# Kernel optimization log

Hardware: AMD Instinct MI355X
Metric: run time of the kernel (lower is better)

## Reference

```python
import jax, jax.numpy as jnp
import numpy as np

EC = 32        # pos-embed channels per coordinate (gno_embed_channels)
MAXP = 10000.0 # gno_embed_max_positions


def sin_embed(c):
    # c: [N, D] coords in [0,1] -> [N, D*EC] transformer-style sinusoidal embedding
    half = EC // 2
    freqs = MAXP ** (jnp.arange(half, dtype=jnp.float32) / half)
    ang = c[..., None] * freqs                       # [N, D, half]
    emb = jnp.concatenate([jnp.sin(ang), jnp.cos(ang)], axis=-1)  # [N, D, EC]
    return emb.reshape(c.shape[0], -1)


def mlp(h, layers):
    n = len(layers)
    for i, (W, b) in enumerate(layers):
        h = h @ W + b
        if i < n - 1:
            h = jax.nn.gelu(h)
    return h


def gno(y, xq, f_y, idx, layers, lift, reduction):
    # y: [n_y,3] source coords, xq: [n_x,3] query coords, f_y: [n_y,C_f], idx: [n_x,K]
    ye, xe = sin_embed(y), sin_embed(xq)
    K = idx.shape[1]
    ef = jnp.concatenate(
        [ye[idx], jnp.broadcast_to(xe[:, None, :], (xq.shape[0], K, xe.shape[-1]))], axis=-1)
    k = mlp(ef, layers)                              # [n_x, K, C] kernel values
    f = f_y if lift is None else f_y @ lift[0] + lift[1]
    msg = k * f[idx]                                 # gathered features modulated by kernel
    return msg.mean(axis=1) if reduction == 'mean' else msg.sum(axis=1)


def spectral_conv(v, w):
    # v: [1,X,Y,Z,C]; w: [4,m,m,m,C,C,2] (4 corner blocks, real/imag stacked)
    m = w.shape[2]
    wc = w[..., 0] + 1j * w[..., 1]
    vf = jnp.fft.rfftn(v, axes=(1, 2, 3))
    out = jnp.zeros_like(vf)
    corners = [(slice(0, m), slice(0, m)), (slice(0, m), slice(-m, None)),
               (slice(-m, None), slice(0, m)), (slice(-m, None), slice(-m, None))]
    for i, (sx, sy) in enumerate(corners):
        blk = jnp.einsum('bxyzi,xyzio->bxyzo', vf[:, sx, sy, :m, :], wc[i])
        out = out.at[:, sx, sy, :m, :].set(blk)
    return jnp.fft.irfftn(out, s=v.shape[1:4], axes=(1, 2, 3))


def _forward(input_geom, latent_queries, output_queries, x,
             in_lift_w, in_lift_b,
             in_k_w0, in_k_b0, in_k_w1, in_k_b1, in_k_w2, in_k_b2, in_k_w3, in_k_b3,
             lift_w0, lift_b0, lift_w1, lift_b1,
             spec_w, skip_w, gate_w, gate_b, cmlp_w0, cmlp_b0, cmlp_w1, cmlp_b1,
             out_k_w0, out_k_b0, out_k_w1, out_k_b1, out_k_w2, out_k_b2,
             proj_w0, proj_b0, proj_w1, proj_b1,
             in_idx, out_idx):
    grid = latent_queries.shape[:-1]
    flat_lq = latent_queries.reshape(-1, latent_queries.shape[-1])
    # --- input GNO: point cloud -> latent grid (mean reduction) ---
    in_layers = [(in_k_w0, in_k_b0), (in_k_w1, in_k_b1), (in_k_w2, in_k_b2), (in_k_w3, in_k_b3)]
    in_p = gno(input_geom, flat_lq, x, in_idx, in_layers, (in_lift_w, in_lift_b), 'mean')
    h = in_p.reshape((1,) + grid + (in_p.shape[-1],))
    # --- lifting ChannelMLP (2 layers) ---
    h = jax.nn.gelu(h @ lift_w0 + lift_b0) @ lift_w1 + lift_b1
    # --- FNO blocks ---
    for l in range(spec_w.shape[0]):
        v_fno = spectral_conv(h, spec_w[l])
        v_skip = h @ skip_w[l]                       # linear skip
        a = jax.nn.gelu(v_fno + v_skip)
        gate = a * gate_w[l] + gate_b[l]             # soft-gating skip
        m_ = jax.nn.gelu(a @ cmlp_w0[l] + cmlp_b0[l]) @ cmlp_w1[l] + cmlp_b1[l]
        h = jax.nn.gelu(m_ + gate)
    x_latent = h.reshape(-1, h.shape[-1])            # [nx*ny*nz, C]
    # --- output GNO: latent grid -> output queries (sum reduction) ---
    out_layers = [(out_k_w0, out_k_b0), (out_k_w1, out_k_b1), (out_k_w2, out_k_b2)]
    out_eval = gno(flat_lq, output_queries, x_latent, out_idx, out_layers, None, 'sum')
    out = out_eval[None]                             # [1, n_out, C]
    # --- projection ChannelMLP ---
    return jax.nn.gelu(out @ proj_w0 + proj_b0) @ proj_w1 + proj_b1


def setup_inputs() -> dict:
    key = jax.random.key(0)
    ks = jax.random.split(key, 24)
    N_IN, N_OUT, G, K = 100000, 30000, 32, 10
    C_IN, H = 3, 64
    KIN = 2 * 3 * EC  # 192: concat of two per-point embeddings

    def w(k, shape, fan):
        return jax.random.normal(k, shape, jnp.float32) / np.sqrt(fan)

    lin = jnp.linspace(0.0, 1.0, G)
    gx, gy, gz = jnp.meshgrid(lin, lin, lin, indexing='ij')
    d = {
        'input_geom': jax.random.uniform(ks[0], (N_IN, 3), jnp.float32),
        'latent_queries': jnp.stack([gx, gy, gz], axis=-1),
        'output_queries': jax.random.uniform(ks[1], (N_OUT, 3), jnp.float32),
        'x': jax.random.normal(ks[2], (N_IN, C_IN), jnp.float32),
        'in_lift_w': w(ks[3], (C_IN, H), C_IN), 'in_lift_b': jnp.zeros((H,)),
        'in_k_w0': w(ks[4], (KIN, 80), KIN), 'in_k_b0': jnp.zeros((80,)),
        'in_k_w1': w(ks[5], (80, 80), 80), 'in_k_b1': jnp.zeros((80,)),
        'in_k_w2': w(ks[6], (80, 80), 80), 'in_k_b2': jnp.zeros((80,)),
        'in_k_w3': w(ks[7], (80, H), 80), 'in_k_b3': jnp.zeros((H,)),
        'lift_w0': w(ks[8], (H, 128), H), 'lift_b0': jnp.zeros((128,)),
        'lift_w1': w(ks[9], (128, H), 128), 'lift_b1': jnp.zeros((H,)),
        'spec_w': jax.random.normal(ks[10], (4, 4, 8, 8, 8, H, H, 2), jnp.float32) * 0.02,
        'skip_w': w(ks[11], (4, H, H), H),
        'gate_w': jnp.ones((4, H)), 'gate_b': jnp.zeros((4, H)),
        'cmlp_w0': w(ks[12], (4, H, 128), H), 'cmlp_b0': jnp.zeros((4, 128)),
        'cmlp_w1': w(ks[13], (4, 128, H), 128), 'cmlp_b1': jnp.zeros((4, H)),
        'out_k_w0': w(ks[14], (KIN, 512), KIN), 'out_k_b0': jnp.zeros((512,)),
        'out_k_w1': w(ks[15], (512, 256), 512), 'out_k_b1': jnp.zeros((256,)),
        'out_k_w2': w(ks[16], (256, H), 256), 'out_k_b2': jnp.zeros((H,)),
        'proj_w0': w(ks[17], (H, 256), H), 'proj_b0': jnp.zeros((256,)),
        'proj_w1': w(ks[18], (256, 1), 256), 'proj_b1': jnp.zeros((1,)),
        'in_idx': jax.random.randint(ks[19], (G ** 3, K), 0, N_IN),
        'out_idx': jax.random.randint(ks[20], (N_OUT, K), 0, G ** 3),
    }
    return d


def reference(input_geom, latent_queries, output_queries, x,
              in_lift_w, in_lift_b,
              in_k_w0, in_k_b0, in_k_w1, in_k_b1, in_k_w2, in_k_b2, in_k_w3, in_k_b3,
              lift_w0, lift_b0, lift_w1, lift_b1,
              spec_w, skip_w, gate_w, gate_b, cmlp_w0, cmlp_b0, cmlp_w1, cmlp_b1,
              out_k_w0, out_k_b0, out_k_w1, out_k_b1, out_k_w2, out_k_b2,
              proj_w0, proj_b0, proj_w1, proj_b1,
              in_idx, out_idx):
    return _forward(input_geom, latent_queries, output_queries, x,
                    in_lift_w, in_lift_b,
                    in_k_w0, in_k_b0, in_k_w1, in_k_b1, in_k_w2, in_k_b2, in_k_w3, in_k_b3,
                    lift_w0, lift_b0, lift_w1, lift_b1,
                    spec_w, skip_w, gate_w, gate_b, cmlp_w0, cmlp_b0, cmlp_w1, cmlp_b1,
                    out_k_w0, out_k_b0, out_k_w1, out_k_b1, out_k_w2, out_k_b2,
                    proj_w0, proj_b0, proj_w1, proj_b1,
                    in_idx, out_idx)
```

## Files before the change

### kernel.cpp

```cpp
#include <hip/hip_runtime.h>
#include <math.h>

#define N_IN   100000
#define N_LQ   32768
#define N_OUT  30000
#define KNB    10

typedef _Float16 h8 __attribute__((ext_vector_type(8)));
typedef _Float16 h4 __attribute__((ext_vector_type(4)));
typedef float    v4f __attribute__((ext_vector_type(4)));

__device__ __forceinline__ float gelu_f(float x){
  float t = 0.79788456080286536f * (x + 0.044715f*x*x*x);
  t = fminf(fmaxf(t, -15.f), 15.f);
  float e = __expf(2.f*t);
  float th = __fdividef(e - 1.f, e + 1.f);
  return 0.5f*x*(1.f + th);
}

__device__ __forceinline__ void barrier_lds(){
  __builtin_amdgcn_s_waitcnt(0xC07F);
  __builtin_amdgcn_s_barrier();
}

__global__ void k_twiddle(float* __restrict__ twc, float* __restrict__ tws){
  int t = threadIdx.x;
  if(t < 32){
    double a = (double)t * 0.19634954084936207;
    twc[t] = (float)cos(a);
    tws[t] = (float)sin(a);
  }
}

__global__ void k_prep(const float* __restrict__ okw1, const float* __restrict__ okw2,
                       const float* __restrict__ ikw1, const float* __restrict__ ikw2,
                       const float* __restrict__ ikw3,
                       _Float16* W1h, _Float16* W1l, _Float16* W2h, _Float16* W2l,
                       _Float16* I1h, _Float16* I1l, _Float16* I2h, _Float16* I2l,
                       _Float16* I3h, _Float16* I3l)
{
  int idx = blockIdx.x*256 + threadIdx.x;
  if(idx < 512*256){
    int k = idx>>8, n = idx&255;
    float v = okw1[idx];
    _Float16 hi = (_Float16)v;
    W1h[n*512+k] = hi; W1l[n*512+k] = (_Float16)((v-(float)hi)*2048.f);
  }
  if(idx < 256*64){
    int k = idx>>6, n = idx&63;
    float v = okw2[idx];
    _Float16 hi = (_Float16)v;
    W2h[n*256+k] = hi; W2l[n*256+k] = (_Float16)((v-(float)hi)*2048.f);
  }
  if(idx < 6400){
    int n = idx/80, k = idx - n*80;
    float v = ikw1[k*80+n];
    _Float16 hi = (_Float16)v;
    I1h[n*80+k] = hi; I1l[n*80+k] = (_Float16)((v-(float)hi)*2048.f);
    float v2 = ikw2[k*80+n];
    _Float16 hi2 = (_Float16)v2;
    I2h[n*80+k] = hi2; I2l[n*80+k] = (_Float16)((v2-(float)hi2)*2048.f);
  }
  if(idx < 5120){
    int n = idx/80, k = idx - n*80;
    float v = ikw3[k*64+n];
    _Float16 hi = (_Float16)v;
    I3h[n*80+k] = hi; I3l[n*80+k] = (_Float16)((v-(float)hi)*2048.f);
  }
}

__global__ void k_lift_in(const float* __restrict__ x, const float* __restrict__ w,
                          const float* __restrict__ b, float* __restrict__ f){
  int i = blockIdx.x*256 + threadIdx.x;
  if(i >= N_IN*64) return;
  int p = i>>6, c = i&63;
  float v = b[c];
  v = fmaf(x[p*3+0], w[c],      v);
  v = fmaf(x[p*3+1], w[64+c],   v);
  v = fmaf(x[p*3+2], w[128+c],  v);
  f[i] = v;
}

template<int COLS, bool BIAS>
__global__ __launch_bounds__(256) void k_embed_partial(
    const float* __restrict__ coords, int npts,
    const float* __restrict__ W, int roff,
    const float* __restrict__ bias, float* __restrict__ outp)
{
  __shared__ float emb[96*8];
  int p0 = blockIdx.x*8;
  int t  = threadIdx.x;
  for(int w = t; w < 384; w += 256){
    int pl = w / 48, s = w - pl*48;
    int d = s >> 4, fi = s & 15;
    int p = p0 + pl;
    float cd = (p < npts) ? coords[(size_t)p*3 + d] : 0.f;
    double f = exp((double)fi * 0.5756462732485115);
    double a = (double)cd * f;
    double sn, cs; sincos(a, &sn, &cs);
    emb[((d<<5)+fi)*8 + pl]      = (float)sn;
    emb[((d<<5)+16+fi)*8 + pl]   = (float)cs;
  }
  __syncthreads();
  for(int c = t; c < COLS; c += 256){
    float acc[8];
    float bb = BIAS ? bias[c] : 0.f;
    #pragma unroll
    for(int u=0;u<8;u++) acc[u] = bb;
    for(int i=0;i<96;i++){
      float wv = W[(size_t)(roff+i)*COLS + c];
      const float* ep = &emb[i*8];
      float4 e0 = *(const float4*)ep;
      float4 e1 = *(const float4*)(ep+4);
      acc[0]=fmaf(e0.x,wv,acc[0]); acc[1]=fmaf(e0.y,wv,acc[1]);
      acc[2]=fmaf(e0.z,wv,acc[2]); acc[3]=fmaf(e0.w,wv,acc[3]);
      acc[4]=fmaf(e1.x,wv,acc[4]); acc[5]=fmaf(e1.y,wv,acc[5]);
      acc[6]=fmaf(e1.z,wv,acc[6]); acc[7]=fmaf(e1.w,wv,acc[7]);
    }
    #pragma unroll
    for(int u=0;u<8;u++){
      int p = p0+u;
      if(p < npts) outp[(size_t)p*COLS + c] = acc[u];
    }
  }
}

#define GI_HAHI 0
#define GI_HALO 5632
#define GI_WHI  11264
#define GI_WLO  14464
__global__ __launch_bounds__(256,2) void k_gino(
    const float* __restrict__ Ain, const float* __restrict__ Bin,
    const float* __restrict__ f_in, const int* __restrict__ iidx,
    const _Float16* __restrict__ I1h, const _Float16* __restrict__ I1l, const float* __restrict__ b1,
    const _Float16* __restrict__ I2h, const _Float16* __restrict__ I2l, const float* __restrict__ b2,
    const _Float16* __restrict__ I3h, const _Float16* __restrict__ I3l, const float* __restrict__ b3,
    float* __restrict__ in_p)
{
  __shared__ _Float16 SG[17664];
  __shared__ int js[64]; __shared__ int qs[64];
  int t = threadIdx.x;
  int wid = t>>6, lane = t&63, quad = lane>>4, lm = lane&15;
  int et0 = blockIdx.x*64;
  if(t<64){ js[t] = iidx[et0+t]; qs[t] = (et0+t)/KNB; }
  barrier_lds();

  {
    int e = t>>2, k4 = t&3;
    size_t ja = (size_t)js[e]*80, qa = (size_t)qs[e]*80;
    #pragma unroll
    for(int u=0;u<3;u++){
      int kl = k4*8 + u*32;
      if(kl < 80){
        float4 a0 = *(const float4*)(Ain + ja + kl);
        float4 a1 = *(const float4*)(Ain + ja + kl + 4);
        float4 c0 = *(const float4*)(Bin + qa + kl);
        float4 c1 = *(const float4*)(Bin + qa + kl + 4);
        float vv[8] = {a0.x+c0.x, a0.y+c0.y, a0.z+c0.z, a0.w+c0.w,
                       a1.x+c1.x, a1.y+c1.y, a1.z+c1.z, a1.w+c1.w};
        h8 hh, ll;
        #pragma unroll
        for(int q8=0;q8<8;q8++){
          float g = gelu_f(vv[q8]);
          _Float16 hi = (_Float16)g;
          hh[q8] = hi; ll[q8] = (_Float16)((g-(float)hi)*2048.f);
        }
        *(h8*)&SG[GI_HAHI + e*88 + kl] = hh;
        *(h8*)&SG[GI_HALO + e*88 + kl] = ll;
      }
    }
  }

  const float inv = 4.8828125e-4f;
  const _Float16* whp[3] = {I1h, I2h, I3h};
  const _Float16* wlp[3] = {I1l, I2l, I3l};
  const float*    bsp[3] = {b1, b2, b3};
  v4f aH[5], aL[5];

  for(int l=0;l<3;l++){
    int NT = (l==2)?4:5;
    const _Float16* wh = whp[l];
    const _Float16* wl = wlp[l];
    #pragma unroll
    for(int n=0;n<5;n++){ aH[n] = (v4f)(0.f); aL[n] = (v4f)(0.f); }
    for(int c=0;c<3;c++){
      int kb = c*32;
      int per = (c==2)?2:4;
      int units = NT*16*per;
      barrier_lds();
      for(int u=t; u<units; u+=256){
        int n = u/per, kh = (u - n*per)*8;
        float4 rh = *(const float4*)(wh + n*80 + kb + kh);
        float4 rl = *(const float4*)(wl + n*80 + kb + kh);
        *(float4*)&SG[GI_WHI + n*40 + kh] = rh;
        *(float4*)&SG[GI_WLO + n*40 + kh] = rl;
      }
      barrier_lds();
      int arow = (wid*16+lm)*88;
      if(c<2){
        h8 ah = *(const h8*)&SG[GI_HAHI + arow + kb + quad*8];
        h8 al = *(const h8*)&SG[GI_HALO + arow + kb + quad*8];
        for(int n=0;n<NT;n++){
          int brow = (n*16+lm)*40;
          h8 bh = *(const h8*)&SG[GI_WHI + brow + quad*8];
          h8 bl = *(const h8*)&SG[GI_WLO + brow + quad*8];
          aH[n] = __builtin_amdgcn_mfma_f32_16x16x32_f16(ah, bh, aH[n], 0,0,0);
          aL[n] = __builtin_amdgcn_mfma_f32_16x16x32_f16(ah, bl, aL[n], 0,0,0);
          aL[n] = __builtin_amdgcn_mfma_f32_16x16x32_f16(al, bh, aL[n], 0,0,0);
        }
      } else {
        h4 ah = *(const h4*)&SG[GI_HAHI + arow + 64 + quad*4];
        h4 al = *(const h4*)&SG[GI_HALO + arow + 64 + quad*4];
        for(int n=0;n<NT;n++){
          int brow = (n*16+lm)*40;
          h4 bh = *(const h4*)&SG[GI_WHI + brow + quad*4];
          h4 bl = *(const h4*)&SG[GI_WLO + brow + quad*4];
          aH[n] = __builtin_amdgcn_mfma_f32_16x16x16f16(ah, bh, aH[n], 0,0,0);
          aL[n] = __builtin_amdgcn_mfma_f32_16x16x16f16(ah, bl, aL[n], 0,0,0);
          aL[n] = __builtin_amdgcn_mfma_f32_16x16x16f16(al, bh, aL[n], 0,0,0);
        }
      }
    }
    if(l<2){
      for(int n=0;n<NT;n++){
        float bb = bsp[l][n*16+lm];
        #pragma unroll
        for(int reg=0;reg<4;reg++){
          int e = wid*16 + quad*4 + reg;
          float v = aH[n][reg] + aL[n][reg]*inv + bb;
          v = gelu_f(v);
          _Float16 hi = (_Float16)v;
          SG[GI_HAHI + e*88 + n*16+lm] = hi;
          SG[GI_HALO + e*88 + n*16+lm] = (_Float16)((v-(float)hi)*2048.f);
        }
      }
    } else {
      for(int n=0;n<NT;n++){
        int col = n*16+lm;
        float bb = bsp[2][col];
        #pragma unroll
        for(int reg=0;reg<4;reg++){
          int e = wid*16 + quad*4 + reg;
          float v = aH[n][reg] + aL[n][reg]*inv + bb;
          v *= f_in[(size_t)js[e]*64 + col] * 0.1f;
          atomicAdd(&in_p[(size_t)qs[e]*64 + col], v);
        }
      }
    }
  }
}

__global__ __launch_bounds__(256,2) void k_ogno(
    const float* __restrict__ Aout, const float* __restrict__ Bout,
    const int* __restrict__ oidx,
    const _Float16* __restrict__ W1h, const _Float16* __restrict__ W1l,
    const float* __restrict__ b1,
    const _Float16* __restrict__ W2h, const _Float16* __restrict__ W2l,
    const float* __restrict__ b2,
    const float* __restrict__ xlat, float* __restrict__ outev, int eEnd)
{
  __shared__ _Float16 SH[33792];
  __shared__ int js[64]; __shared__ int qs[64];
  int t = threadIdx.x;
  int wid = t>>6, lane = t&63, quad = lane>>4, lm = lane&15;
  int et0 = blockIdx.x*64;
  if(t<64){
    int ec = et0+t; if(ec >= eEnd) ec = eEnd-1;
    js[t] = oidx[ec]; qs[t] = ec/KNB;
  }
  barrier_lds();

  v4f accH[4][4], accL[4][4];
  #pragma unroll
  for(int m=0;m<4;m++)
    #pragma unroll
    for(int n=0;n<4;n++){ accH[m][n] = (v4f)(0.f); accL[m][n] = (v4f)(0.f); }

  int se = t>>2, skl = (t&3)*8;
  const float* pa = Aout + (size_t)js[se]*512 + skl;
  const float* pb = Bout + (size_t)qs[se]*512 + skl;

  float4 cA0 = *(const float4*)(pa);
  float4 cA1 = *(const float4*)(pa+4);
  float4 cB0 = *(const float4*)(pb);
  float4 cB1 = *(const float4*)(pb+4);

  #pragma unroll 1
  for(int kk=0; kk<512; kk+=32){
    int base = ((kk>>5)&1)*5120;
    {
      float vv[8] = {cA0.x+cB0.x, cA0.y+cB0.y, cA0.z+cB0.z, cA0.w+cB0.w,
                     cA1.x+cB1.x, cA1.y+cB1.y, cA1.z+cB1.z, cA1.w+cB1.w};
      h8 hh, ll;
      #pragma unroll
      for(int q8=0;q8<8;q8++){
        float g = gelu_f(vv[q8]);
        _Float16 hi = (_Float16)g;
        hh[q8] = hi; ll[q8] = (_Float16)((g-(float)hi)*2048.f);
      }
      *(h8*)&SH[base + se*40 + skl] = hh;
      *(h8*)&SH[base + 2560 + se*40 + skl] = ll;
    }
    barrier_lds();
    if(kk < 480){
      cA0 = *(const float4*)(pa + kk + 32);
      cA1 = *(const float4*)(pa + kk + 36);
      cB0 = *(const float4*)(pb + kk + 32);
      cB1 = *(const float4*)(pb + kk + 36);
    }
    h8 bh[4], bl[4];
    #pragma unroll
    for(int n=0;n<4;n++){
      size_t off = (size_t)((wid*4+n)*16+lm)*512 + kk + quad*8;
      bh[n] = *(const h8*)(W1h + off);
      bl[n] = *(const h8*)(W1l + off);
    }
    h8 ah[4], al[4];
    #pragma unroll
    for(int m=0;m<4;m++){
      ah[m] = *(const h8*)&SH[base + (m*16+lm)*40 + quad*8];
      al[m] = *(const h8*)&SH[base + 2560 + (m*16+lm)*40 + quad*8];
    }
    #pragma unroll
    for(int n=0;n<4;n++)
      #pragma unroll
      for(int m=0;m<4;m++)
        accH[m][n] = __builtin_amdgcn_mfma_f32_16x16x32_f16(ah[m], bh[n], accH[m][n], 0,0,0);
    #pragma unroll
    for(int n=0;n<4;n++)
      #pragma unroll
      for(int m=0;m<4;m++)
        accL[m][n] = __builtin_amdgcn_mfma_f32_16x16x32_f16(ah[m], bl[n], accL[m][n], 0,0,0);
    #pragma unroll
    for(int n=0;n<4;n++)
      #pragma unroll
      for(int m=0;m<4;m++)
        accL[m][n] = __builtin_amdgcn_mfma_f32_16x16x32_f16(al[m], bh[n], accL[m][n], 0,0,0);
  }
  barrier_lds();

  const float inv = 4.8828125e-4f;
  #pragma unroll
  for(int n=0;n<4;n++){
    int col = (wid*4+n)*16 + lm;
    float bb = b1[col];
    #pragma unroll
    for(int m=0;m<4;m++){
      #pragma unroll
      for(int reg=0;reg<4;reg++){
        int e = m*16 + quad*4 + reg;
        float v = accH[m][n][reg] + accL[m][n][reg]*inv + bb;
        v = gelu_f(v);
        _Float16 hi = (_Float16)v;
        SH[e*264 + col] = hi;
        SH[16896 + e*264 + col] = (_Float16)((v-(float)hi)*2048.f);
      }
    }
  }
  barrier_lds();

  v4f acc2H[4], acc2L[4];
  #pragma unroll
  for(int m=0;m<4;m++){ acc2H[m] = (v4f)(0.f); acc2L[m] = (v4f)(0.f); }
  int n2 = wid*16 + lm;
  #pragma unroll
  for(int c=0;c<8;c++){
    int ksub = c*32;
    size_t woff = (size_t)n2*256 + ksub + quad*8;
    h8 bh2 = *(const h8*)(W2h + woff);
    h8 bl2 = *(const h8*)(W2l + woff);
    #pragma unroll
    for(int m=0;m<4;m++){
      h8 a2h = *(const h8*)&SH[(m*16+lm)*264 + ksub + quad*8];
      h8 a2l = *(const h8*)&SH[16896 + (m*16+lm)*264 + ksub + quad*8];
      acc2H[m] = __builtin_amdgcn_mfma_f32_16x16x32_f16(a2h, bh2, acc2H[m], 0,0,0);
      acc2L[m] = __builtin_amdgcn_mfma_f32_16x16x32_f16(a2h, bl2, acc2L[m], 0,0,0);
      acc2L[m] = __builtin_amdgcn_mfma_f32_16x16x32_f16(a2l, bh2, acc2L[m], 0,0,0);
    }
  }

  float bb2 = b2[n2];
  #pragma unroll
  for(int m=0;m<4;m++){
    #pragma unroll
    for(int reg=0;reg<4;reg++){
      int e = m*16 + quad*4 + reg;
      int eg = et0 + e;
      if(eg < eEnd){
        float v = acc2H[m][reg] + acc2L[m][reg]*inv + bb2;
        v *= xlat[(size_t)js[e]*64 + n2];
        atomicAdd(&outev[(size_t)qs[e]*64 + n2], v);
      }
    }
  }
}

__global__ __launch_bounds__(256) void k_mlp_plain(const float* __restrict__ X,
    const float* __restrict__ W0, const float* __restrict__ b0,
    const float* __restrict__ W1, const float* __restrict__ b1,
    float* __restrict__ Y)
{
  __shared__ float xt[64*16];
  __shared__ float ht[128*16];
  int t = threadIdx.x, r0 = blockIdx.x*16;
  for(int w=t; w<1024; w+=256){ int r=w>>6, c=w&63; xt[c*16+r] = X[(size_t)(r0+r)*64+c]; }
  __syncthreads();
  {
    int hc = t & 127, rg = t >> 7;
    float acc[8]; float bb = b0[hc];
    #pragma unroll
    for(int u=0;u<8;u++) acc[u]=bb;
    for(int i=0;i<64;i++){
      float wv = W0[i*128+hc];
      const float* xp = &xt[i*16 + rg*8];
      float4 x0 = *(const float4*)xp; float4 x1 = *(const float4*)(xp+4);
      acc[0]=fmaf(x0.x,wv,acc[0]); acc[1]=fmaf(x0.y,wv,acc[1]);
      acc[2]=fmaf(x0.z,wv,acc[2]); acc[3]=fmaf(x0.w,wv,acc[3]);
      acc[4]=fmaf(x1.x,wv,acc[4]); acc[5]=fmaf(x1.y,wv,acc[5]);
      acc[6]=fmaf(x1.z,wv,acc[6]); acc[7]=fmaf(x1.w,wv,acc[7]);
    }
    #pragma unroll
    for(int u=0;u<8;u++) ht[hc*16 + rg*8 + u] = gelu_f(acc[u]);
  }
  __syncthreads();
  {
    int oc = t & 63, rg = t >> 6;
    float acc2[4]; float bb = b1[oc];
    #pragma unroll
    for(int u=0;u<4;u++) acc2[u]=bb;
    for(int i=0;i<128;i++){
      float wv = W1[i*64+oc];
      float4 h4v = *(const float4*)&ht[i*16 + rg*4];
      acc2[0]=fmaf(h4v.x,wv,acc2[0]); acc2[1]=fmaf(h4v.y,wv,acc2[1]);
      acc2[2]=fmaf(h4v.z,wv,acc2[2]); acc2[3]=fmaf(h4v.w,wv,acc2[3]);
    }
    #pragma unroll
    for(int u=0;u<4;u++) Y[(size_t)(r0+rg*4+u)*64 + oc] = acc2[u];
  }
}

__global__ __launch_bounds__(256) void k_mlp_gated(const float* __restrict__ X,
    const float* __restrict__ W0, const float* __restrict__ b0,
    const float* __restrict__ W1, const float* __restrict__ b1,
    const float* __restrict__ gwp, const float* __restrict__ gbp,
    float* __restrict__ Y)
{
  __shared__ float xt[64*16];
  __shared__ float ht[128*16];
  int t = threadIdx.x, r0 = blockIdx.x*16;
  for(int w=t; w<1024; w+=256){ int r=w>>6, c=w&63; xt[c*16+r] = X[(size_t)(r0+r)*64+c]; }
  __syncthreads();
  {
    int hc = t & 127, rg = t >> 7;
    float acc[8]; float bb = b0[hc];
    #pragma unroll
    for(int u=0;u<8;u++) acc[u]=bb;
    for(int i=0;i<64;i++){
      float wv = W0[i*128+hc];
      const float* xp = &xt[i*16 + rg*8];
      float4 x0 = *(const float4*)xp; float4 x1 = *(const float4*)(xp+4);
      acc[0]=fmaf(x0.x,wv,acc[0]); acc[1]=fmaf(x0.y,wv,acc[1]);
      acc[2]=fmaf(x0.z,wv,acc[2]); acc[3]=fmaf(x0.w,wv,acc[3]);
      acc[4]=fmaf(x1.x,wv,acc[4]); acc[5]=fmaf(x1.y,wv,acc[5]);
      acc[6]=fmaf(x1.z,wv,acc[6]); acc[7]=fmaf(x1.w,wv,acc[7]);
    }
    #pragma unroll
    for(int u=0;u<8;u++) ht[hc*16 + rg*8 + u] = gelu_f(acc[u]);
  }
  __syncthreads();
  {
    int oc = t & 63, rg = t >> 6;
    float acc2[4]; float bb = b1[oc];
    #pragma unroll
    for(int u=0;u<4;u++) acc2[u]=bb;
    for(int i=0;i<128;i++){
      float wv = W1[i*64+oc];
      float4 h4v = *(const float4*)&ht[i*16 + rg*4];
      acc2[0]=fmaf(h4v.x,wv,acc2[0]); acc2[1]=fmaf(h4v.y,wv,acc2[1]);
      acc2[2]=fmaf(h4v.z,wv,acc2[2]); acc2[3]=fmaf(h4v.w,wv,acc2[3]);
    }
    float gwv = gwp[oc], gbv = gbp[oc];
    #pragma unroll
    for(int u=0;u<4;u++){
      int r = rg*4+u;
      float a = xt[oc*16 + r];
      Y[(size_t)(r0+r)*64 + oc] = gelu_f(acc2[u] + fmaf(a, gwv, gbv));
    }
  }
}

__global__ void k_fz_fwd(const float* __restrict__ h, const float* __restrict__ twc,
                         const float* __restrict__ tws, float* __restrict__ Fr, float* __restrict__ Fi){
  int idx = blockIdx.x*256 + threadIdx.x;
  int c = idx&63, kz=(idx>>6)&7, y=(idx>>9)&31, x=idx>>14;
  const float* hp = h + ((size_t)(x*32+y)*32)*64 + c;
  float re=0.f, im=0.f;
  for(int z=0; z<32; z++){
    float v = hp[(size_t)z*64];
    int k = (kz*z)&31;
    re = fmaf(v, twc[k], re);
    im = fmaf(-v, tws[k], im);
  }
  Fr[idx]=re; Fi[idx]=im;
}

__global__ void k_fy_fwd(const float* __restrict__ Ar, const float* __restrict__ Ai,
                         const float* __restrict__ twc, const float* __restrict__ tws,
                         float* __restrict__ Fr, float* __restrict__ Fi){
  int idx = blockIdx.x*256 + threadIdx.x;
  int c = idx&63, kz=(idx>>6)&7, my=(idx>>9)&15, x=idx>>13;
  int ky = my<8 ? my : my+16;
  const float* pr = Ar + ((size_t)(x*32)*8+kz)*64 + c;
  const float* pi = Ai + ((size_t)(x*32)*8+kz)*64 + c;
  float re=0.f, im=0.f;
  for(int y=0;y<32;y++){
    float a = pr[(size_t)y*512], b = pi[(size_t)y*512];
    int k = (ky*y)&31; float cs=twc[k], sn=tws[k];
    re += a*cs + b*sn;
    im += b*cs - a*sn;
  }
  Fr[idx]=re; Fi[idx]=im;
}

__global__ void k_fx_fwd(const float* __restrict__ Ar, const float* __restrict__ Ai,
                         const float* __restrict__ twc, const float* __restrict__ tws,
                         float* __restrict__ Fr, float* __restrict__ Fi){
  int idx = blockIdx.x*256 + threadIdx.x;
  int c = idx&63, kz=(idx>>6)&7, my=(idx>>9)&15, mx=idx>>13;
  int kx = mx<8 ? mx : mx+16;
  const float* pr = Ar + ((size_t)my*8+kz)*64 + c;
  const float* pi = Ai + ((size_t)my*8+kz)*64 + c;
  float re=0.f, im=0.f;
  for(int x=0;x<32;x++){
    float a = pr[(size_t)x*8192], b = pi[(size_t)x*8192];
    int k = (kx*x)&31; float cs=twc[k], sn=tws[k];
    re += a*cs + b*sn;
    im += b*cs - a*sn;
  }
  Fr[idx]=re; Fi[idx]=im;
}

__global__ void k_smm(const float* __restrict__ Fr, const float* __restrict__ Fi,
                      const float* __restrict__ wlayer,
                      float* __restrict__ Gr, float* __restrict__ Gi){
  int t = threadIdx.x;
  int sub = t>>6, c = t&63;
  int mp = blockIdx.x*4 + sub;
  int kz = mp&7, my=(mp>>3)&15, mx=mp>>7;
  int corner = ((mx>=8)?2:0) | ((my>=8)?1:0);
  int kxp = mx&7, kyp = my&7;
  const float* wp = wlayer + (size_t)(((corner*8+kxp)*8+kyp)*8+kz)*8192;
  __shared__ float fre[4][64], fim[4][64];
  fre[sub][c] = Fr[(size_t)mp*64+c];
  fim[sub][c] = Fi[(size_t)mp*64+c];
  __syncthreads();
  float are=0.f, aim=0.f;
  for(int i=0;i<64;i++){
    float2 wv = *(const float2*)&wp[(size_t)(i*64+c)*2];
    float a = fre[sub][i], b = fim[sub][i];
    are += a*wv.x - b*wv.y;
    aim += a*wv.y + b*wv.x;
  }
  Gr[(size_t)mp*64+c] = are;
  Gi[(size_t)mp*64+c] = aim;
}

__global__ void k_fx_inv(const float* __restrict__ Ar, const float* __restrict__ Ai,
                         const float* __restrict__ twc, const float* __restrict__ tws,
                         float* __restrict__ Fr, float* __restrict__ Fi){
  int idx = blockIdx.x*256 + threadIdx.x;
  int c = idx&63, kz=(idx>>6)&7, my=(idx>>9)&15, x=idx>>13;
  float re=0.f, im=0.f;
  for(int mx=0;mx<16;mx++){
    int kx = mx<8 ? mx : mx+16;
    int k = (kx*x)&31; float cs=twc[k], sn=tws[k];
    float a = Ar[(size_t)((mx*16+my)*8+kz)*64+c];
    float b = Ai[(size_t)((mx*16+my)*8+kz)*64+c];
    re += a*cs - b*sn;
    im += a*sn + b*cs;
  }
  Fr[idx]=re; Fi[idx]=im;
}

__global__ void k_fy_inv(const float* __restrict__ Ar, const float* __restrict__ Ai,
                         const float* __restrict__ twc, const float* __restrict__ tws,
                         float* __restrict__ Fr, float* __restrict__ Fi){
  int idx = blockIdx.x*256 + threadIdx.x;
  int c = idx&63, kz=(idx>>6)&7, y=(idx>>9)&31, x=idx>>14;
  float re=0.f, im=0.f;
  for(int my=0;my<16;my++){
    int ky = my<8 ? my : my+16;
    int k = (ky*y)&31; float cs=twc[k], sn=tws[k];
    float a = Ar[(size_t)((x*16+my)*8+kz)*64+c];
    float b = Ai[(size_t)((x*16+my)*8+kz)*64+c];
    re += a*cs - b*sn;
    im += a*sn + b*cs;
  }
  Fr[idx]=re; Fi[idx]=im;
}

__global__ void k_fz_inv_skip(const float* __restrict__ G2re, const float* __restrict__ G2im,
    const float* __restrict__ h, const float* __restrict__ twc, const float* __restrict__ tws,
    const float* __restrict__ sw, float* __restrict__ a_out)
{
  __shared__ float hrow[4][64];
  int t = threadIdx.x; int c = t&63; int pl = t>>6;
  int p = blockIdx.x*4 + pl;
  int z = p & 31; int xy = p >> 5;
  hrow[pl][c] = h[(size_t)p*64 + c];
  __syncthreads();
  const float* gr = G2re + (size_t)(xy*8)*64 + c;
  const float* gi = G2im + (size_t)(xy*8)*64 + c;
  float acc = gr[0];
  #pragma unroll
  for(int kz=1;kz<8;kz++){
    int k = (kz*z)&31;
    acc += 2.f*(gr[(size_t)kz*64]*twc[k] - gi[(size_t)kz*64]*tws[k]);
  }
  float vfno = acc * (1.f/32768.f);
  float vskip = 0.f;
  for(int i=0;i<64;i++) vskip = fmaf(hrow[pl][i], sw[i*64+c], vskip);
  a_out[(size_t)p*64+c] = gelu_f(vfno + vskip);
}

__global__ __launch_bounds__(256) void k_proj(const float* __restrict__ outev,
    const float* __restrict__ pw0, const float* __restrict__ pb0,
    const float* __restrict__ pw1, const float* __restrict__ pb1,
    float* __restrict__ outp)
{
  __shared__ float msg[8][64];
  __shared__ float red[8][4];
  int t = threadIdx.x; int q0 = blockIdx.x*8;
  for(int w=t; w<512; w+=256){
    int qq=w>>6, o=w&63; int q=q0+qq;
    msg[qq][o] = (q<N_OUT) ? outev[(size_t)q*64+o] : 0.f;
  }
  __syncthreads();
  float p[8]; float bb = pb0[t];
  #pragma unroll
  for(int qq=0;qq<8;qq++) p[qq]=bb;
  for(int o=0;o<64;o++){
    float wv = pw0[o*256+t];
    #pragma unroll
    for(int qq=0;qq<8;qq++) p[qq] = fmaf(msg[qq][o], wv, p[qq]);
  }
  float w1v = pw1[t];
  int lane = t & 63, wid = t >> 6;
  #pragma unroll
  for(int qq=0;qq<8;qq++){
    float v = gelu_f(p[qq]) * w1v;
    for(int d=32; d>=1; d>>=1) v += __shfl_down(v, d, 64);
    if(lane==0) red[qq][wid]=v;
  }
  __syncthreads();
  if(t<8){
    int q = q0+t;
    if(q<N_OUT) outp[q] = red[t][0]+red[t][1]+red[t][2]+red[t][3] + pb1[0];
  }
}

extern "C" void kernel_launch(void* const* d_in, const int* in_sizes, int n_in,
                              void* d_out, int out_size, void* d_ws, size_t ws_size,
                              hipStream_t stream)
{
  (void)in_sizes; (void)n_in; (void)out_size; (void)ws_size;
  const float* geom = (const float*)d_in[0];
  const float* latq = (const float*)d_in[1];
  const float* outq = (const float*)d_in[2];
  const float* xin  = (const float*)d_in[3];
  const float* ilw  = (const float*)d_in[4];
  const float* ilb  = (const float*)d_in[5];
  const float* ikw0 = (const float*)d_in[6];
  const float* ikb0 = (const float*)d_in[7];
  const float* ikw1 = (const float*)d_in[8];
  const float* ikb1 = (const float*)d_in[9];
  const float* ikw2 = (const float*)d_in[10];
  const float* ikb2 = (const float*)d_in[11];
  const float* ikw3 = (const float*)d_in[12];
  const float* ikb3 = (const float*)d_in[13];
  const float* lw0  = (const float*)d_in[14];
  const float* lb0  = (const float*)d_in[15];
  const float* lw1  = (const float*)d_in[16];
  const float* lb1  = (const float*)d_in[17];
  const float* specw= (const float*)d_in[18];
  const float* skw  = (const float*)d_in[19];
  const float* gw   = (const float*)d_in[20];
  const float* gb   = (const float*)d_in[21];
  const float* cw0  = (const float*)d_in[22];
  const float* cb0  = (const float*)d_in[23];
  const float* cw1  = (const float*)d_in[24];
  const float* cb1  = (const float*)d_in[25];
  const float* okw0 = (const float*)d_in[26];
  const float* okb0 = (const float*)d_in[27];
  const float* okw1 = (const float*)d_in[28];
  const float* okb1 = (const float*)d_in[29];
  const float* okw2 = (const float*)d_in[30];
  const float* okb2 = (const float*)d_in[31];
  const float* pw0  = (const float*)d_in[32];
  const float* pb0  = (const float*)d_in[33];
  const float* pw1  = (const float*)d_in[34];
  const float* pb1  = (const float*)d_in[35];
  const int* iidx = (const int*)d_in[36];
  const int* oidx = (const int*)d_in[37];
  float* outp = (float*)d_out;
  float* ws = (float*)d_ws;

  size_t off = 0;
  float* F_IN = ws + off; off += (size_t)N_IN*64;
  float* AIN  = ws + off; off += (size_t)N_IN*80;
  float* BIN_ = ws + off; off += (size_t)N_LQ*80;
  float* AOUT = ws + off; off += (size_t)N_LQ*512;
  float* BOUT = ws + off; off += (size_t)N_OUT*512;
  float* HBUF = ws + off; off += (size_t)N_LQ*64;
  float* ABUF = ws + off; off += (size_t)N_LQ*64;
  float* FZr = ws+off; off+=524288; float* FZi = ws+off; off+=524288;
  float* FYr = ws+off; off+=262144; float* FYi = ws+off; off+=262144;
  float* FXr = ws+off; off+=131072; float* FXi = ws+off; off+=131072;
  float* GMr = ws+off; off+=131072; float* GMi = ws+off; off+=131072;
  float* G1r = ws+off; off+=262144; float* G1i = ws+off; off+=262144;
  float* G2r = ws+off; off+=524288; float* G2i = ws+off; off+=524288;
  float* OUTEV = ws+off; off += (size_t)N_OUT*64;
  float* TWC = ws+off; off+=32; float* TWS = ws+off; off+=32;
  off = (off + 3) & ~(size_t)3;
  _Float16* P = (_Float16*)(ws + off);
  _Float16 *W1h = P,          *W1l = P+131072;
  _Float16 *W2h = P+262144,   *W2l = P+278528;
  _Float16 *I1h = P+294912,   *I1l = P+301312;
  _Float16 *I2h = P+307712,   *I2l = P+314112;
  _Float16 *I3h = P+320512,   *I3l = P+325632;

  k_twiddle<<<1, 64, 0, stream>>>(TWC, TWS);
  k_prep<<<512, 256, 0, stream>>>(okw1, okw2, ikw1, ikw2, ikw3,
                                  W1h, W1l, W2h, W2l, I1h, I1l, I2h, I2l, I3h, I3l);
  k_lift_in<<<(N_IN*64)/256, 256, 0, stream>>>(xin, ilw, ilb, F_IN);
  k_embed_partial<80,false><<<N_IN/8, 256, 0, stream>>>(geom, N_IN, ikw0, 0, (const float*)nullptr, AIN);
  k_embed_partial<80,true ><<<N_LQ/8, 256, 0, stream>>>(latq, N_LQ, ikw0, 96, ikb0, BIN_);
  k_embed_partial<512,false><<<N_LQ/8, 256, 0, stream>>>(latq, N_LQ, okw0, 0, (const float*)nullptr, AOUT);
  k_embed_partial<512,true ><<<(N_OUT+7)/8, 256, 0, stream>>>(outq, N_OUT, okw0, 96, okb0, BOUT);

  hipMemsetAsync(HBUF, 0, (size_t)N_LQ*64*sizeof(float), stream);
  k_gino<<<(N_LQ*KNB)/64, 256, 0, stream>>>(AIN, BIN_, F_IN, iidx,
                                            I1h, I1l, ikb1, I2h, I2l, ikb2, I3h, I3l, ikb3, HBUF);
  k_mlp_plain<<<N_LQ/16, 256, 0, stream>>>(HBUF, lw0, lb0, lw1, lb1, HBUF);

  for(int l=0;l<4;l++){
    k_fz_fwd<<<2048,256,0,stream>>>(HBUF, TWC, TWS, FZr, FZi);
    k_fy_fwd<<<1024,256,0,stream>>>(FZr, FZi, TWC, TWS, FYr, FYi);
    k_fx_fwd<<<512,256,0,stream>>>(FYr, FYi, TWC, TWS, FXr, FXi);
    k_smm<<<512,256,0,stream>>>(FXr, FXi, specw + (size_t)l*16777216, GMr, GMi);
    k_fx_inv<<<1024,256,0,stream>>>(GMr, GMi, TWC, TWS, G1r, G1i);
    k_fy_inv<<<2048,256,0,stream>>>(G1r, G1i, TWC, TWS, G2r, G2i);
    k_fz_inv_skip<<<8192,256,0,stream>>>(G2r, G2i, HBUF, TWC, TWS, skw + (size_t)l*4096, ABUF);
    k_mlp_gated<<<N_LQ/16,256,0,stream>>>(ABUF, cw0 + (size_t)l*8192, cb0 + l*128,
                                          cw1 + (size_t)l*8192, cb1 + l*64,
                                          gw + l*64, gb + l*64, HBUF);
  }

  hipMemsetAsync(OUTEV, 0, (size_t)N_OUT*64*sizeof(float), stream);
  k_ogno<<<(N_OUT*KNB + 63)/64, 256, 0, stream>>>(AOUT, BOUT, oidx,
                                                  W1h, W1l, okb1, W2h, W2l, okb2,
                                                  HBUF, OUTEV, N_OUT*KNB);
  k_proj<<<(N_OUT+7)/8, 256, 0, stream>>>(OUTEV, pw0, pb0, pw1, pb1, outp);
}
```

Measured before the change: 1.873 ms.

## Shrink k_ogno LDS footprint and software-prefetch W1 fragments across iterations

The second MLP layer in k_ogno now runs one 16-row slice at a time, so the shared staging buffer shrinks from about 66KB to 20KB, which could allow more resident blocks per CU. W1 fragments and the next A/B activation chunks are prefetched into registers one iteration ahead, and the K-loop is unrolled by 2. W2 fragments are held in registers for the whole second stage. Dropping the min-2-blocks launch bound frees the register budget, which risks spills or lower occupancy from more VGPR pressure. The row-sliced second stage also adds barriers.

```diff
diff --git a/kernel.cpp b/kernel.cpp
--- a/kernel.cpp
+++ b/kernel.cpp
@@ -250,7 +250,7 @@
   }
 }
 
-__global__ __launch_bounds__(256,2) void k_ogno(
+__global__ __launch_bounds__(256) void k_ogno(
     const float* __restrict__ Aout, const float* __restrict__ Bout,
     const int* __restrict__ oidx,
     const _Float16* __restrict__ W1h, const _Float16* __restrict__ W1l,
@@ -259,7 +259,7 @@
     const float* __restrict__ b2,
     const float* __restrict__ xlat, float* __restrict__ outev, int eEnd)
 {
-  __shared__ _Float16 SH[33792];
+  __shared__ _Float16 SH[10240];
   __shared__ int js[64]; __shared__ int qs[64];
   int t = threadIdx.x;
   int wid = t>>6, lane = t&63, quad = lane>>4, lm = lane&15;
@@ -279,13 +279,20 @@
   int se = t>>2, skl = (t&3)*8;
   const float* pa = Aout + (size_t)js[se]*512 + skl;
   const float* pb = Bout + (size_t)qs[se]*512 + skl;
+  size_t wbase = (size_t)((wid*4)*16+lm)*512 + quad*8;
 
   float4 cA0 = *(const float4*)(pa);
   float4 cA1 = *(const float4*)(pa+4);
   float4 cB0 = *(const float4*)(pb);
   float4 cB1 = *(const float4*)(pb+4);
-
-  #pragma unroll 1
+  h8 cwh[4], cwl[4];
+  #pragma unroll
+  for(int n=0;n<4;n++){
+    cwh[n] = *(const h8*)(W1h + wbase + (size_t)n*16*512);
+    cwl[n] = *(const h8*)(W1l + wbase + (size_t)n*16*512);
+  }
+
+  #pragma unroll 2
   for(int kk=0; kk<512; kk+=32){
     int base = ((kk>>5)&1)*5120;
     {
@@ -302,18 +309,16 @@
       *(h8*)&SH[base + 2560 + se*40 + skl] = ll;
     }
     barrier_lds();
-    if(kk < 480){
-      cA0 = *(const float4*)(pa + kk + 32);
-      cA1 = *(const float4*)(pa + kk + 36);
-      cB0 = *(const float4*)(pb + kk + 32);
-      cB1 = *(const float4*)(pb + kk + 36);
-    }
-    h8 bh[4], bl[4];
+    int kn = (kk < 480) ? kk + 32 : kk;
+    float4 nA0 = *(const float4*)(pa + kn);
+    float4 nA1 = *(const float4*)(pa + kn + 4);
+    float4 nB0 = *(const float4*)(pb + kn);
+    float4 nB1 = *(const float4*)(pb + kn + 4);
+    h8 nwh[4], nwl[4];
     #pragma unroll
     for(int n=0;n<4;n++){
-      size_t off = (size_t)((wid*4+n)*16+lm)*512 + kk + quad*8;
-      bh[n] = *(const h8*)(W1h + off);
-      bl[n] = *(const h8*)(W1l + off);
+      nwh[n] = *(const h8*)(W1h + wbase + (size_t)n*16*512 + kn);
+      nwl[n] = *(const h8*)(W1l + wbase + (size_t)n*16*512 + kn);
     }
     h8 ah[4], al[4];
     #pragma unroll
@@ -325,69 +330,69 @@
     for(int n=0;n<4;n++)
       #pragma unroll
       for(int m=0;m<4;m++)
-        accH[m][n] = __builtin_amdgcn_mfma_f32_16x16x32_f16(ah[m], bh[n], accH[m][n], 0,0,0);
+        accH[m][n] = __builtin_amdgcn_mfma_f32_16x16x32_f16(ah[m], cwh[n], accH[m][n], 0,0,0);
     #pragma unroll
     for(int n=0;n<4;n++)
       #pragma unroll
       for(int m=0;m<4;m++)
-        accL[m][n] = __builtin_amdgcn_mfma_f32_16x16x32_f16(ah[m], bl[n], accL[m][n], 0,0,0);
+        accL[m][n] = __builtin_amdgcn_mfma_f32_16x16x32_f16(ah[m], cwl[n], accL[m][n], 0,0,0);
     #pragma unroll
     for(int n=0;n<4;n++)
       #pragma unroll
       for(int m=0;m<4;m++)
-        accL[m][n] = __builtin_amdgcn_mfma_f32_16x16x32_f16(al[m], bh[n], accL[m][n], 0,0,0);
-  }
-  barrier_lds();
+        accL[m][n] = __builtin_amdgcn_mfma_f32_16x16x32_f16(al[m], cwh[n], accL[m][n], 0,0,0);
+    cA0 = nA0; cA1 = nA1; cB0 = nB0; cB1 = nB1;
+    #pragma unroll
+    for(int n=0;n<4;n++){ cwh[n] = nwh[n]; cwl[n] = nwl[n]; }
+  }
 
   const float inv = 4.8828125e-4f;
+  int n2 = wid*16 + lm;
+  h8 w2h_r[8], w2l_r[8];
   #pragma unroll
-  for(int n=0;n<4;n++){
-    int col = (wid*4+n)*16 + lm;
-    float bb = b1[col];
-    #pragma unroll
-    for(int m=0;m<4;m++){
+  for(int c=0;c<8;c++){
+    size_t woff = (size_t)n2*256 + c*32 + quad*8;
+    w2h_r[c] = *(const h8*)(W2h + woff);
+    w2l_r[c] = *(const h8*)(W2l + woff);
+  }
+  float b1c[4];
+  #pragma unroll
+  for(int n=0;n<4;n++) b1c[n] = b1[(wid*4+n)*16 + lm];
+  float bb2 = b2[n2];
+
+  #pragma unroll 1
+  for(int m=0;m<4;m++){
+    barrier_lds();
+    #pragma unroll
+    for(int n=0;n<4;n++){
+      int col = (wid*4+n)*16 + lm;
       #pragma unroll
       for(int reg=0;reg<4;reg++){
-        int e = m*16 + quad*4 + reg;
-        float v = accH[m][n][reg] + accL[m][n][reg]*inv + bb;
+        int r16 = quad*4 + reg;
+        float v = accH[m][n][reg] + accL[m][n][reg]*inv + b1c[n];
         v = gelu_f(v);
         _Float16 hi = (_Float16)v;
-        SH[e*264 + col] = hi;
-        SH[16896 + e*264 + col] = (_Float16)((v-(float)hi)*2048.f);
+        SH[r16*264 + col] = hi;
+        SH[4224 + r16*264 + col] = (_Float16)((v-(float)hi)*2048.f);
       }
     }
-  }
-  barrier_lds();
-
-  v4f acc2H[4], acc2L[4];
-  #pragma unroll
-  for(int m=0;m<4;m++){ acc2H[m] = (v4f)(0.f); acc2L[m] = (v4f)(0.f); }
-  int n2 = wid*16 + lm;
-  #pragma unroll
-  for(int c=0;c<8;c++){
-    int ksub = c*32;
-    size_t woff = (size_t)n2*256 + ksub + quad*8;
-    h8 bh2 = *(const h8*)(W2h + woff);
-    h8 bl2 = *(const h8*)(W2l + woff);
-    #pragma unroll
-    for(int m=0;m<4;m++){
-      h8 a2h = *(const h8*)&SH[(m*16+lm)*264 + ksub + quad*8];
-      h8 a2l = *(const h8*)&SH[16896 + (m*16+lm)*264 + ksub + quad*8];
-      acc2H[m] = __builtin_amdgcn_mfma_f32_16x16x32_f16(a2h, bh2, acc2H[m], 0,0,0);
-      acc2L[m] = __builtin_amdgcn_mfma_f32_16x16x32_f16(a2h, bl2, acc2L[m], 0,0,0);
-      acc2L[m] = __builtin_amdgcn_mfma_f32_16x16x32_f16(a2l, bh2, acc2L[m], 0,0,0);
-    }
-  }
-
-  float bb2 = b2[n2];
-  #pragma unroll
-  for(int m=0;m<4;m++){
+    barrier_lds();
+    v4f a2H = (v4f)(0.f), a2L = (v4f)(0.f);
+    #pragma unroll
+    for(int c=0;c<8;c++){
+      int ksub = c*32;
+      h8 a2h = *(const h8*)&SH[lm*264 + ksub + quad*8];
+      h8 a2l = *(const h8*)&SH[4224 + lm*264 + ksub + quad*8];
+      a2H = __builtin_amdgcn_mfma_f32_16x16x32_f16(a2h, w2h_r[c], a2H, 0,0,0);
+      a2L = __builtin_amdgcn_mfma_f32_16x16x32_f16(a2h, w2l_r[c], a2L, 0,0,0);
+      a2L = __builtin_amdgcn_mfma_f32_16x16x32_f16(a2l, w2h_r[c], a2L, 0,0,0);
+    }
     #pragma unroll
     for(int reg=0;reg<4;reg++){
       int e = m*16 + quad*4 + reg;
       int eg = et0 + e;
       if(eg < eEnd){
-        float v = acc2H[m][reg] + acc2L[m][reg]*inv + bb2;
+        float v = a2H[reg] + a2L[reg]*inv + bb2;
         v *= xlat[(size_t)js[e]*64 + n2];
         atomicAdd(&outev[(size_t)qs[e]*64 + n2], v);
       }
```

After: 2.204 ms. +17.7%, slower.
